# Performance work log

Measured on AMD Instinct MI355X. Metric: run time of the kernel, lower is better.

Reference implementation:

```python
import jax, jax.numpy as jnp
import numpy as np

N = 40000      # nodes
E = 640000     # edges (avg degree 16)
F_IN = 33      # input residue features (hard-coded in module)
H = 128        # hidden_channels
C_OUT = 3      # output classes (hard-coded)
L = 8          # num_layers
ALPHA = 0.1
THETA = 0.5


def setup_inputs() -> dict:
    key = jax.random.key(0)
    ks = jax.random.split(key, 8)
    x = jax.random.normal(ks[0], (N, F_IN), jnp.float32)
    edge_row = jax.random.randint(ks[1], (E,), 0, N)
    edge_col = jax.random.randint(ks[2], (E,), 0, N)
    edge_weight = jax.random.uniform(ks[3], (E,), jnp.float32)
    # nn.Linear stores weight as [out, in]
    W_in = jax.random.normal(ks[4], (H, F_IN), jnp.float32) * 0.1
    b_in = jnp.zeros((H,), jnp.float32)
    W_out = jax.random.normal(ks[5], (C_OUT, H), jnp.float32) * 0.1
    b_out = jnp.zeros((C_OUT,), jnp.float32)
    # GCN2Conv shared weight1 per layer: [L, H, H]
    W_conv = jax.random.normal(ks[6], (L, H, H), jnp.float32) * (1.0 / np.sqrt(H))
    return dict(x=x, edge_row=edge_row, edge_col=edge_col, edge_weight=edge_weight,
                W_in=W_in, b_in=b_in, W_out=W_out, b_out=b_out, W_conv=W_conv)


def reference(x, edge_row, edge_col, edge_weight, W_in, b_in, W_out, b_out, W_conv):
    # dropout p=0.0 -> identity (also eval mode)
    x0 = jax.nn.relu(x @ W_in.T + b_in)                      # [N, H]
    # GCN2Conv beta_l = log(theta / layer + 1), layer = 1..L
    betas = jnp.log(THETA / jnp.arange(1.0, L + 1.0, dtype=jnp.float32) + 1.0)

    def spmm(h):
        # adj_t @ h : gather source-node features, weight, scatter-add to rows
        return jax.ops.segment_sum(edge_weight[:, None] * h[edge_col], edge_row,
                                   num_segments=N)

    def step(xc, lw):
        W, beta = lw
        # GCN2Conv (shared_weights=True, normalize=False):
        #   xx = (1-alpha)*A@h + alpha*x0 ; out = (1-beta)*xx + beta*(xx@W)
        xx = (1.0 - ALPHA) * spmm(xc) + ALPHA * x0
        out = (1.0 - beta) * xx + beta * (xx @ W)
        return xc + jax.nn.relu(out), None                   # residual in GCN.forward

    x_final, _ = jax.lax.scan(step, x0, (W_conv, betas))
    return x_final @ W_out.T + b_out                          # [N, 3]
```

## Files before the change

kernel.cpp:

```cpp
#include <hip/hip_runtime.h>
#include <hip/hip_bf16.h>
#include <math.h>

#define N_NODES 40000
#define NE      640000
#define FIN     33
#define H       128
#define COUT    3
#define NLAYERS 8
#define ALPHA   0.1f
#define THETA   0.5f
#define CAP     96

#define SB_SCAT 625
#define SB_WPRE 512
#define SB_XIN  2500

typedef __bf16 bf16x8 __attribute__((ext_vector_type(8)));
typedef float  f32x4  __attribute__((ext_vector_type(4)));

__device__ inline unsigned short f2bf(float f) {
    __hip_bfloat16 b = __float2bfloat16(f);
    return *(unsigned short*)&b;
}
__device__ inline float bf2f(unsigned short u) {
    __hip_bfloat16 b = *(__hip_bfloat16*)&u;
    return __bfloat162float(b);
}

__global__ __launch_bounds__(256) void k_setup(
        const int* __restrict__ row, const int* __restrict__ col,
        const float* __restrict__ w, int* __restrict__ cnt,
        unsigned int* __restrict__ bucket,
        const float* __restrict__ Wconv, unsigned short* __restrict__ Wtbf,
        const float* __restrict__ x, const float* __restrict__ Win,
        const float* __restrict__ bin,
        unsigned short* __restrict__ x0bf, unsigned short* __restrict__ hbf) {
    __shared__ float sW[H * FIN];
    __shared__ float sx[16][FIN];
    int b = blockIdx.x, t = threadIdx.x;

    if (b < SB_SCAT) {
        int e0 = (b * 256 + t) * 4;
        int r[4], pos[4];
        unsigned int rec[4];
        #pragma unroll
        for (int i = 0; i < 4; i++) {
            int e = e0 + i;
            r[i] = row[e];
            unsigned int wb = f2bf((1.0f - ALPHA) * w[e]);
            rec[i] = (wb << 16) | (unsigned int)col[e];
        }
        #pragma unroll
        for (int i = 0; i < 4; i++) pos[i] = atomicAdd(&cnt[r[i]], 1);
        #pragma unroll
        for (int i = 0; i < 4; i++) bucket[(size_t)r[i] * CAP + pos[i]] = rec[i];
        return;
    }
    if (b < SB_SCAT + SB_WPRE) {
        int idx = (b - SB_SCAT) * 256 + t;
        int l = idx >> 14;
        int rem = idx & 16383;
        int k = rem >> 7, j = rem & 127;
        float beta = logf(THETA / (float)(l + 1) + 1.0f);
        float v = beta * Wconv[idx];
        if (j == k) v += 1.0f - beta;
        Wtbf[l * 16384 + j * 128 + k] = f2bf(v);
        return;
    }
    {
        int n0 = (b - SB_SCAT - SB_WPRE) * 16;
        for (int i = t; i < H * FIN; i += 256) sW[i] = Win[i];
        for (int i = t; i < 16 * FIN; i += 256)
            sx[i / FIN][i % FIN] = x[(size_t)(n0 + i / FIN) * FIN + (i % FIN)];
        __syncthreads();
        int f = t % H;
        int l0 = t / H;
        float bv = bin[f];
        for (int lo = l0; lo < 16; lo += 2) {
            float acc = bv;
            #pragma unroll
            for (int k = 0; k < FIN; k++) acc += sx[lo][k] * sW[f * FIN + k];
            acc = fmaxf(acc, 0.f);
            size_t idx = (size_t)(n0 + lo) * H + f;
            unsigned short bb = f2bf(acc);
            x0bf[idx] = bb;
            hbf[idx] = bb;
        }
    }
}

__global__ __launch_bounds__(256) void k_spmm(const int* __restrict__ cnt,
                       const unsigned int* __restrict__ bucket,
                       const unsigned short* __restrict__ hbf,
                       const unsigned short* __restrict__ x0bf,
                       unsigned short* __restrict__ xxbf) {
    int wave = (blockIdx.x * blockDim.x + threadIdx.x) >> 6;
    int lane = threadIdx.x & 63;
    if (wave >= N_NODES) return;
    int deg = cnt[wave];
    const unsigned int* ep = bucket + (size_t)wave * CAP;
    int slot = lane >> 4;
    int fid  = lane & 15;

    float acc[8] = {0,0,0,0,0,0,0,0};

    for (int e = 0; e < deg; e += 16) {
        unsigned int u[4];
        uint4 q[4];
        #pragma unroll
        for (int k = 0; k < 4; k++) {
            int ei = e + k * 4 + slot;
            unsigned int uu = ep[ei];
            u[k] = (ei < deg) ? uu : 0u;
        }
        #pragma unroll
        for (int k = 0; k < 4; k++)
            q[k] = *(const uint4*)(hbf + (size_t)(u[k] & 0xffffu) * H + fid * 8);
        #pragma unroll
        for (int k = 0; k < 4; k++) {
            float w = bf2f((unsigned short)(u[k] >> 16));
            acc[0] += w * bf2f((unsigned short)(q[k].x & 0xffffu));
            acc[1] += w * bf2f((unsigned short)(q[k].x >> 16));
            acc[2] += w * bf2f((unsigned short)(q[k].y & 0xffffu));
            acc[3] += w * bf2f((unsigned short)(q[k].y >> 16));
            acc[4] += w * bf2f((unsigned short)(q[k].z & 0xffffu));
            acc[5] += w * bf2f((unsigned short)(q[k].z >> 16));
            acc[6] += w * bf2f((unsigned short)(q[k].w & 0xffffu));
            acc[7] += w * bf2f((unsigned short)(q[k].w >> 16));
        }
    }

    #pragma unroll
    for (int j = 0; j < 8; j++) {
        acc[j] += __shfl_xor(acc[j], 16);
        acc[j] += __shfl_xor(acc[j], 32);
    }

    if (slot == 0) {
        uint4 xq = *(const uint4*)(x0bf + (size_t)wave * H + fid * 8);
        float o0 = acc[0] + ALPHA * bf2f((unsigned short)(xq.x & 0xffffu));
        float o1 = acc[1] + ALPHA * bf2f((unsigned short)(xq.x >> 16));
        float o2 = acc[2] + ALPHA * bf2f((unsigned short)(xq.y & 0xffffu));
        float o3 = acc[3] + ALPHA * bf2f((unsigned short)(xq.y >> 16));
        float o4 = acc[4] + ALPHA * bf2f((unsigned short)(xq.z & 0xffffu));
        float o5 = acc[5] + ALPHA * bf2f((unsigned short)(xq.z >> 16));
        float o6 = acc[6] + ALPHA * bf2f((unsigned short)(xq.w & 0xffffu));
        float o7 = acc[7] + ALPHA * bf2f((unsigned short)(xq.w >> 16));
        uint4 r;
        r.x = (unsigned int)f2bf(o0) | ((unsigned int)f2bf(o1) << 16);
        r.y = (unsigned int)f2bf(o2) | ((unsigned int)f2bf(o3) << 16);
        r.z = (unsigned int)f2bf(o4) | ((unsigned int)f2bf(o5) << 16);
        r.w = (unsigned int)f2bf(o6) | ((unsigned int)f2bf(o7) << 16);
        *(uint4*)(xxbf + (size_t)wave * H + fid * 8) = r;
    }
}

__global__ __launch_bounds__(128) void k_gemm(const unsigned short* __restrict__ xxbf,
                       const unsigned short* __restrict__ Wtbf,
                       unsigned short* __restrict__ hbf,
                       const float* __restrict__ Wout, const float* __restrict__ bout,
                       float* __restrict__ out, int do_out) {
    int t = threadIdx.x;
    int wv = t >> 6, lane = t & 63;
    int quad = lane >> 4, l16 = lane & 15;
    int rbase = blockIdx.x * 32 + wv * 16;

    f32x4 acc[8];
    #pragma unroll
    for (int j = 0; j < 8; j++) acc[j] = (f32x4){0.f, 0.f, 0.f, 0.f};

    #pragma unroll
    for (int k0 = 0; k0 < 4; k0++) {
        bf16x8 av = *(const bf16x8*)(xxbf + (size_t)(rbase + l16) * H + k0 * 32 + quad * 8);
        #pragma unroll
        for (int j = 0; j < 8; j++) {
            bf16x8 bv = *(const bf16x8*)(Wtbf + (size_t)(j * 16 + l16) * H + k0 * 32 + quad * 8);
            acc[j] = __builtin_amdgcn_mfma_f32_16x16x32_bf16(av, bv, acc[j], 0, 0, 0);
        }
    }

    float po[4][3];
    #pragma unroll
    for (int r = 0; r < 4; r++) { po[r][0] = 0.f; po[r][1] = 0.f; po[r][2] = 0.f; }

    #pragma unroll
    for (int j = 0; j < 8; j++) {
        int col = j * 16 + l16;
        float w0 = 0.f, w1 = 0.f, w2 = 0.f;
        if (do_out) { w0 = Wout[col]; w1 = Wout[H + col]; w2 = Wout[2 * H + col]; }
        #pragma unroll
        for (int r = 0; r < 4; r++) {
            int row = rbase + quad * 4 + r;
            size_t idx = (size_t)row * H + col;
            float hv = bf2f(hbf[idx]) + fmaxf(acc[j][r], 0.f);
            hbf[idx] = f2bf(hv);
            po[r][0] += hv * w0; po[r][1] += hv * w1; po[r][2] += hv * w2;
        }
    }

    if (do_out) {
        #pragma unroll
        for (int off = 1; off < 16; off <<= 1) {
            #pragma unroll
            for (int r = 0; r < 4; r++) {
                po[r][0] += __shfl_xor(po[r][0], off);
                po[r][1] += __shfl_xor(po[r][1], off);
                po[r][2] += __shfl_xor(po[r][2], off);
            }
        }
        if (l16 == 0) {
            #pragma unroll
            for (int r = 0; r < 4; r++) {
                int row = rbase + quad * 4 + r;
                out[(size_t)row * 3 + 0] = po[r][0] + bout[0];
                out[(size_t)row * 3 + 1] = po[r][1] + bout[1];
                out[(size_t)row * 3 + 2] = po[r][2] + bout[2];
            }
        }
    }
}

extern "C" void kernel_launch(void* const* d_in, const int* in_sizes, int n_in,
                              void* d_out, int out_size, void* d_ws, size_t ws_size,
                              hipStream_t stream) {
    const float* x     = (const float*)d_in[0];
    const int*   erow  = (const int*)  d_in[1];
    const int*   ecol  = (const int*)  d_in[2];
    const float* ew    = (const float*)d_in[3];
    const float* Win   = (const float*)d_in[4];
    const float* bin   = (const float*)d_in[5];
    const float* Wout  = (const float*)d_in[6];
    const float* bout  = (const float*)d_in[7];
    const float* Wconv = (const float*)d_in[8];
    float* out = (float*)d_out;

    char* ws = (char*)d_ws;
    const size_t NHb = (size_t)N_NODES * H * sizeof(unsigned short);
    unsigned short* xxbf  = (unsigned short*)(ws);
    unsigned short* x0bf  = (unsigned short*)(ws + NHb);
    unsigned short* hbf   = (unsigned short*)(ws + 2 * NHb);
    char* p = ws + 3 * NHb;
    unsigned short* Wtbf  = (unsigned short*)p;  p += 8 * H * H * 2;
    int*  cnt     = (int*) p;  p += 160256;
    unsigned int* bucket = (unsigned int*)p;

    hipMemsetAsync(cnt, 0, (size_t)N_NODES * 4, stream);
    k_setup<<<SB_SCAT + SB_WPRE + SB_XIN, 256, 0, stream>>>(
        erow, ecol, ew, cnt, bucket, Wconv, Wtbf, x, Win, bin, x0bf, hbf);

    for (int l = 0; l < NLAYERS; l++) {
        k_spmm<<<N_NODES / 4,  256, 0, stream>>>(cnt, bucket, hbf, x0bf, xxbf);
        k_gemm<<<N_NODES / 32, 128, 0, stream>>>(xxbf, Wtbf + (size_t)l * H * H,
                                                 hbf, Wout, bout, out,
                                                 (l == NLAYERS - 1) ? 1 : 0);
    }
}
```

Baseline: 459.3 us.

## Fuse all layers into one persistent cooperative kernel with grid syncs

```diff
diff --git a/kernel.cpp b/kernel.cpp
--- a/kernel.cpp
+++ b/kernel.cpp
@@ -1,6 +1,9 @@
 #include <hip/hip_runtime.h>
 #include <hip/hip_bf16.h>
+#include <hip/hip_cooperative_groups.h>
 #include <math.h>
+
+namespace cg = cooperative_groups;
 
 #define N_NODES 40000
 #define NE      640000
@@ -15,6 +18,10 @@
 #define SB_SCAT 625
 #define SB_WPRE 512
 #define SB_XIN  2500
+
+#define PBLK    512
+#define NWAVE   (PBLK * 4)
+#define NTILE   (N_NODES / 16)
 
 typedef __bf16 bf16x8 __attribute__((ext_vector_type(8)));
 typedef float  f32x4  __attribute__((ext_vector_type(4)));
@@ -90,6 +97,163 @@
     }
 }
 
+__device__ inline void gemm_tile(int rbase, int quad, int l16,
+        const unsigned short* __restrict__ xxbf, const unsigned short* __restrict__ Wl,
+        unsigned short* __restrict__ hbf, float (&h)[8][4], bool last,
+        const float* __restrict__ Wout, const float* __restrict__ bout,
+        float* __restrict__ out) {
+    f32x4 acc[8];
+    #pragma unroll
+    for (int j = 0; j < 8; j++) acc[j] = (f32x4){0.f, 0.f, 0.f, 0.f};
+    #pragma unroll
+    for (int k0 = 0; k0 < 4; k0++) {
+        bf16x8 av = *(const bf16x8*)(xxbf + (size_t)(rbase + l16) * H + k0 * 32 + quad * 8);
+        #pragma unroll
+        for (int j = 0; j < 8; j++) {
+            bf16x8 bv = *(const bf16x8*)(Wl + (size_t)(j * 16 + l16) * H + k0 * 32 + quad * 8);
+            acc[j] = __builtin_amdgcn_mfma_f32_16x16x32_bf16(av, bv, acc[j], 0, 0, 0);
+        }
+    }
+    if (!last) {
+        #pragma unroll
+        for (int j = 0; j < 8; j++) {
+            int col = j * 16 + l16;
+            #pragma unroll
+            for (int r = 0; r < 4; r++) {
+                h[j][r] += fmaxf(acc[j][r], 0.f);
+                hbf[(size_t)(rbase + quad * 4 + r) * H + col] = f2bf(h[j][r]);
+            }
+        }
+    } else {
+        float po[4][3];
+        #pragma unroll
+        for (int r = 0; r < 4; r++) { po[r][0] = 0.f; po[r][1] = 0.f; po[r][2] = 0.f; }
+        #pragma unroll
+        for (int j = 0; j < 8; j++) {
+            int col = j * 16 + l16;
+            float w0 = Wout[col], w1 = Wout[H + col], w2 = Wout[2 * H + col];
+            #pragma unroll
+            for (int r = 0; r < 4; r++) {
+                float hv = h[j][r] + fmaxf(acc[j][r], 0.f);
+                po[r][0] += hv * w0; po[r][1] += hv * w1; po[r][2] += hv * w2;
+            }
+        }
+        #pragma unroll
+        for (int off = 1; off < 16; off <<= 1) {
+            #pragma unroll
+            for (int r = 0; r < 4; r++) {
+                po[r][0] += __shfl_xor(po[r][0], off);
+                po[r][1] += __shfl_xor(po[r][1], off);
+                po[r][2] += __shfl_xor(po[r][2], off);
+            }
+        }
+        if (l16 == 0) {
+            #pragma unroll
+            for (int r = 0; r < 4; r++) {
+                int row = rbase + quad * 4 + r;
+                out[(size_t)row * 3 + 0] = po[r][0] + bout[0];
+                out[(size_t)row * 3 + 1] = po[r][1] + bout[1];
+                out[(size_t)row * 3 + 2] = po[r][2] + bout[2];
+            }
+        }
+    }
+}
+
+__global__ __launch_bounds__(256, 2) void k_layers(
+        const int* __restrict__ cnt, const unsigned int* __restrict__ bucket,
+        const unsigned short* __restrict__ x0bf, unsigned short* __restrict__ hbf,
+        unsigned short* __restrict__ xxbf, const unsigned short* __restrict__ Wtbf,
+        const float* __restrict__ Wout, const float* __restrict__ bout,
+        float* __restrict__ out) {
+    cg::grid_group grid = cg::this_grid();
+    int wave_g = (int)((blockIdx.x * 256 + threadIdx.x) >> 6);
+    int lane = threadIdx.x & 63;
+    int slot = lane >> 4, fid = lane & 15;
+    int quad = lane >> 4, l16 = lane & 15;
+
+    int t0 = wave_g;
+    int t1 = wave_g + NWAVE;
+    bool h1v = t1 < NTILE;
+    int rb0 = t0 * 16, rb1 = t1 * 16;
+
+    float h0[8][4], h1[8][4];
+    #pragma unroll
+    for (int j = 0; j < 8; j++)
+        #pragma unroll
+        for (int r = 0; r < 4; r++)
+            h0[j][r] = bf2f(x0bf[(size_t)(rb0 + quad * 4 + r) * H + j * 16 + l16]);
+    if (h1v) {
+        #pragma unroll
+        for (int j = 0; j < 8; j++)
+            #pragma unroll
+            for (int r = 0; r < 4; r++)
+                h1[j][r] = bf2f(x0bf[(size_t)(rb1 + quad * 4 + r) * H + j * 16 + l16]);
+    }
+
+    for (int l = 0; l < NLAYERS; l++) {
+        for (int row = wave_g; row < N_NODES; row += NWAVE) {
+            int deg = cnt[row];
+            const unsigned int* ep = bucket + (size_t)row * CAP;
+            float acc[8] = {0,0,0,0,0,0,0,0};
+            for (int e = 0; e < deg; e += 16) {
+                unsigned int u[4];
+                uint4 q[4];
+                #pragma unroll
+                for (int k = 0; k < 4; k++) {
+                    int ei = e + k * 4 + slot;
+                    unsigned int uu = ep[ei];
+                    u[k] = (ei < deg) ? uu : 0u;
+                }
+                #pragma unroll
+                for (int k = 0; k < 4; k++)
+                    q[k] = *(const uint4*)(hbf + (size_t)(u[k] & 0xffffu) * H + fid * 8);
+                #pragma unroll
+                for (int k = 0; k < 4; k++) {
+                    float w = bf2f((unsigned short)(u[k] >> 16));
+                    acc[0] += w * bf2f((unsigned short)(q[k].x & 0xffffu));
+                    acc[1] += w * bf2f((unsigned short)(q[k].x >> 16));
+                    acc[2] += w * bf2f((unsigned short)(q[k].y & 0xffffu));
+                    acc[3] += w * bf2f((unsigned short)(q[k].y >> 16));
+                    acc[4] += w * bf2f((unsigned short)(q[k].z & 0xffffu));
+                    acc[5] += w * bf2f((unsigned short)(q[k].z >> 16));
+                    acc[6] += w * bf2f((unsigned short)(q[k].w & 0xffffu));
+                    acc[7] += w * bf2f((unsigned short)(q[k].w >> 16));
+                }
+            }
+            #pragma unroll
+            for (int j = 0; j < 8; j++) {
+                acc[j] += __shfl_xor(acc[j], 16);
+                acc[j] += __shfl_xor(acc[j], 32);
+            }
+            if (slot == 0) {
+                uint4 xq = *(const uint4*)(x0bf + (size_t)row * H + fid * 8);
+                float o0 = acc[0] + ALPHA * bf2f((unsigned short)(xq.x & 0xffffu));
+                float o1 = acc[1] + ALPHA * bf2f((unsigned short)(xq.x >> 16));
+                float o2 = acc[2] + ALPHA * bf2f((unsigned short)(xq.y & 0xffffu));
+                float o3 = acc[3] + ALPHA * bf2f((unsigned short)(xq.y >> 16));
+                float o4 = acc[4] + ALPHA * bf2f((unsigned short)(xq.z & 0xffffu));
+                float o5 = acc[5] + ALPHA * bf2f((unsigned short)(xq.z >> 16));
+                float o6 = acc[6] + ALPHA * bf2f((unsigned short)(xq.w & 0xffffu));
+                float o7 = acc[7] + ALPHA * bf2f((unsigned short)(xq.w >> 16));
+                uint4 rr;
+                rr.x = (unsigned int)f2bf(o0) | ((unsigned int)f2bf(o1) << 16);
+                rr.y = (unsigned int)f2bf(o2) | ((unsigned int)f2bf(o3) << 16);
+                rr.z = (unsigned int)f2bf(o4) | ((unsigned int)f2bf(o5) << 16);
+                rr.w = (unsigned int)f2bf(o6) | ((unsigned int)f2bf(o7) << 16);
+                *(uint4*)(xxbf + (size_t)row * H + fid * 8) = rr;
+            }
+        }
+        grid.sync();
+
+        const unsigned short* Wl = Wtbf + (size_t)l * H * H;
+        bool last = (l == NLAYERS - 1);
+        gemm_tile(rb0, quad, l16, xxbf, Wl, hbf, h0, last, Wout, bout, out);
+        if (h1v)
+            gemm_tile(rb1, quad, l16, xxbf, Wl, hbf, h1, last, Wout, bout, out);
+        if (!last) grid.sync();
+    }
+}
+
 __global__ __launch_bounds__(256) void k_spmm(const int* __restrict__ cnt,
                        const unsigned int* __restrict__ bucket,
                        const unsigned short* __restrict__ hbf,
@@ -100,11 +264,8 @@
     if (wave >= N_NODES) return;
     int deg = cnt[wave];
     const unsigned int* ep = bucket + (size_t)wave * CAP;
-    int slot = lane >> 4;
-    int fid  = lane & 15;
-
+    int slot = lane >> 4, fid = lane & 15;
     float acc[8] = {0,0,0,0,0,0,0,0};
-
     for (int e = 0; e < deg; e += 16) {
         unsigned int u[4];
         uint4 q[4];
@@ -130,13 +291,11 @@
             acc[7] += w * bf2f((unsigned short)(q[k].w >> 16));
         }
     }
-
     #pragma unroll
     for (int j = 0; j < 8; j++) {
         acc[j] += __shfl_xor(acc[j], 16);
         acc[j] += __shfl_xor(acc[j], 32);
     }
-
     if (slot == 0) {
         uint4 xq = *(const uint4*)(x0bf + (size_t)wave * H + fid * 8);
         float o0 = acc[0] + ALPHA * bf2f((unsigned short)(xq.x & 0xffffu));
@@ -169,7 +328,6 @@
     f32x4 acc[8];
     #pragma unroll
     for (int j = 0; j < 8; j++) acc[j] = (f32x4){0.f, 0.f, 0.f, 0.f};
-
     #pragma unroll
     for (int k0 = 0; k0 < 4; k0++) {
         bf16x8 av = *(const bf16x8*)(xxbf + (size_t)(rbase + l16) * H + k0 * 32 + quad * 8);
@@ -179,11 +337,9 @@
             acc[j] = __builtin_amdgcn_mfma_f32_16x16x32_bf16(av, bv, acc[j], 0, 0, 0);
         }
     }
-
     float po[4][3];
     #pragma unroll
     for (int r = 0; r < 4; r++) { po[r][0] = 0.f; po[r][1] = 0.f; po[r][2] = 0.f; }
-
     #pragma unroll
     for (int j = 0; j < 8; j++) {
         int col = j * 16 + l16;
@@ -191,14 +347,12 @@
         if (do_out) { w0 = Wout[col]; w1 = Wout[H + col]; w2 = Wout[2 * H + col]; }
         #pragma unroll
         for (int r = 0; r < 4; r++) {
-            int row = rbase + quad * 4 + r;
-            size_t idx = (size_t)row * H + col;
+            size_t idx = (size_t)(rbase + quad * 4 + r) * H + col;
             float hv = bf2f(hbf[idx]) + fmaxf(acc[j][r], 0.f);
             hbf[idx] = f2bf(hv);
             po[r][0] += hv * w0; po[r][1] += hv * w1; po[r][2] += hv * w2;
         }
     }
-
     if (do_out) {
         #pragma unroll
         for (int off = 1; off < 16; off <<= 1) {
@@ -249,10 +403,19 @@
     k_setup<<<SB_SCAT + SB_WPRE + SB_XIN, 256, 0, stream>>>(
         erow, ecol, ew, cnt, bucket, Wconv, Wtbf, x, Win, bin, x0bf, hbf);
 
-    for (int l = 0; l < NLAYERS; l++) {
-        k_spmm<<<N_NODES / 4,  256, 0, stream>>>(cnt, bucket, hbf, x0bf, xxbf);
-        k_gemm<<<N_NODES / 32, 128, 0, stream>>>(xxbf, Wtbf + (size_t)l * H * H,
-                                                 hbf, Wout, bout, out,
-                                                 (l == NLAYERS - 1) ? 1 : 0);
-    }
-}
+    void* args[] = { (void*)&cnt, (void*)&bucket, (void*)&x0bf, (void*)&hbf,
+                     (void*)&xxbf, (void*)&Wtbf, (void*)&Wout, (void*)&bout,
+                     (void*)&out };
+    hipError_t err = hipLaunchCooperativeKernel((const void*)k_layers,
+                                                dim3(PBLK), dim3(256),
+                                                args, 0, stream);
+    if (err != hipSuccess) {
+        (void)hipGetLastError();
+        for (int l = 0; l < NLAYERS; l++) {
+            k_spmm<<<N_NODES / 4,  256, 0, stream>>>(cnt, bucket, hbf, x0bf, xxbf);
+            k_gemm<<<N_NODES / 32, 128, 0, stream>>>(xxbf, Wtbf + (size_t)l * H * H,
+                                                     hbf, Wout, bout, out,
+                                                     (l == NLAYERS - 1) ? 1 : 0);
+        }
+    }
+}
```

After: 1.524 ms. 3.32x slower.
